# Performance work log

Hardware: AMD Instinct MI355X
Metric: run time of the kernel (lower is better)

The kernel has to match this reference:

```python
import jax, jax.numpy as jnp
import numpy as np

B, N_BUG, D_BUG, K, L, P = 2048, 2000, 30, 20, 40, 2
OMEGA_TEMP = 1.0


def setup_inputs() -> dict:
    key = jax.random.key(0)
    ks = jax.random.split(key, 14)
    f = lambda k, s, sc=1.0: sc * jax.random.normal(k, s, dtype=jnp.float32)
    return {
        "x": f(ks[0], (B, N_BUG)),
        "microbe_locs": f(ks[1], (N_BUG, D_BUG)),
        "mu_bug": f(ks[2], (L, D_BUG)),
        "r_bug": jax.random.uniform(ks[3], (L,), dtype=jnp.float32) * 20.0 + 10.0,
        "alpha": f(ks[4], (L, K)),
        "beta": f(ks[5], (K,)),
        "W1": f(ks[6], (K, L, P, 16), 0.5),
        "b1": f(ks[7], (K, L, P, 16), 0.1),
        "W2": f(ks[8], (K, L, P, 16, 16), 0.25),
        "b2": f(ks[9], (K, L, P, 16), 0.1),
        "W3": f(ks[10], (K, L, P, 16, 8), 0.25),
        "b3": f(ks[11], (K, L, P, 8), 0.1),
        "W4": f(ks[12], (K, L, P, 8), 0.35),
        "b4": f(ks[13], (K, L, P), 0.1),
    }


def reference(x, microbe_locs, mu_bug, r_bug, alpha, beta,
              W1, b1, W2, b2, W3, b3, W4, b4):
    # Distance-based soft microbe->cluster assignment (mu/r kernel):
    # kappa[m,l] = ||microbe_locs[m] - mu_bug[l]||^2
    kappa = jnp.sum((microbe_locs[:, None, :] - mu_bug[None, :, :]) ** 2, axis=-1)  # [N_bug, L]
    w_act = jax.nn.sigmoid((r_bug[None, :] - kappa) / OMEGA_TEMP)                  # [N_bug, L]
    g = x @ w_act                                                                   # [B, L] per-cluster microbe sums

    alpha_act = jax.nn.sigmoid(alpha)  # [L, K] soft edge selection

    # NAM: K*L*P independent tiny MLPs 1->16->16->8->1, batched over (k,l,p).
    h1 = jax.nn.elu(g[:, None, :, None, None] * W1[None] + b1[None])          # [B,K,L,P,16]
    h2 = jax.nn.elu(jnp.einsum('bklpi,klpij->bklpj', h1, W2) + b2[None])      # [B,K,L,P,16]
    h3 = jax.nn.elu(jnp.einsum('bklpi,klpij->bklpj', h2, W3) + b3[None])      # [B,K,L,P,8]
    f_out = jnp.einsum('bklpi,klpi->bklp', h3, W4) + b4[None]                 # [B,K,L,P]

    # out[b,k] = beta[k] + sum_l alpha_act[l,k] * sum_p f_out[b,k,l,p]
    out = beta[None, :] + jnp.einsum('bklp,lk->bk', f_out, alpha_act)         # [B,K]
    return out
```

## Files before the change

### kernel.cpp

```cpp
#include <hip/hip_runtime.h>
#include <hip/hip_bf16.h>

#define B_SZ 2048
#define NB   2000
#define DB   30
#define KK   20
#define LL   40
#define PP   2

#define BLOB_F 336

#define GRID_K1 880

typedef _Float16 f16x4 __attribute__((ext_vector_type(4)));
typedef float    f32x4 __attribute__((ext_vector_type(4)));

__device__ __forceinline__ float sigmoidf_fast(float z) {
    return 1.0f / (1.0f + __expf(-z));
}
__device__ __forceinline__ float eluf(float x) {
    return x > 0.0f ? x : (__expf(x) - 1.0f);
}

__global__ __launch_bounds__(256) void k1_prep(
    const float* __restrict__ locs, const float* __restrict__ mu,
    const float* __restrict__ r, const float* __restrict__ alpha,
    const float* __restrict__ beta,
    const float* __restrict__ W1, const float* __restrict__ b1,
    const float* __restrict__ W2, const float* __restrict__ b2,
    const float* __restrict__ W3, const float* __restrict__ b3,
    const float* __restrict__ W4, const float* __restrict__ b4,
    float* __restrict__ w_act, float* __restrict__ blob,
    float* __restrict__ g_T, float* __restrict__ out)
{
    __shared__ float smem[LL * DB + LL];
    const int tid  = threadIdx.x;
    const int bidx = blockIdx.x;
    const int vt   = bidx * 256 + tid;

    for (int j = vt; j < LL * B_SZ; j += GRID_K1 * 256) g_T[j] = 0.0f;

    if (bidx < 320) {
        for (int t = tid; t < LL * DB; t += 256) smem[t] = mu[t];
        if (tid < LL) smem[LL * DB + tid] = r[tid];
        __syncthreads();
        if (vt < NB * LL) {
            int m = vt / LL;
            int l = vt - m * LL;
            float kappa = 0.0f;
            #pragma unroll
            for (int d = 0; d < DB; ++d) {
                float diff = locs[m * DB + d] - smem[l * DB + d];
                kappa += diff * diff;
            }
            w_act[vt] = sigmoidf_fast(smem[LL * DB + l] - kappa);
        }
    } else if (bidx < 720) {
        int vt2 = vt - 320 * 256;
        int bidb = vt2 >> 6;
        int t = vt2 & 63;
        int k = bidb / (PP * LL);
        int rem = bidb - k * (PP * LL);
        int p = rem / LL;
        int l = rem - p * LL;
        int iw = (k * LL + l) * PP + p;
        int n = t & 15, q = t >> 4;
        float* o = blob + (size_t)bidb * BLOB_F;
        float aact = sigmoidf_fast(alpha[l * KK + k]);
        if (t < 16) {
            o[t]      = W1[iw * 16 + t];
            o[16 + t] = b1[iw * 16 + t];
            o[32 + t] = b2[iw * 16 + t];
            o[48 + t] = (t < 8) ? b3[iw * 8 + t] : 0.0f;
            o[64 + t] = (t < 8) ? W4[iw * 8 + t] * aact : 0.0f;
        }
        _Float16* w2a = (_Float16*)(o + 80);
        #pragma unroll
        for (int j = 0; j < 4; ++j)
            w2a[t * 4 + j] = (_Float16)W2[iw * 256 + (4 * q + j) * 16 + n];
        _Float16* w3a = (_Float16*)(o + 208);
        #pragma unroll
        for (int j = 0; j < 4; ++j)
            w3a[t * 4 + j] = (n < 8) ? (_Float16)W3[iw * 128 + (4 * q + j) * 8 + n]
                                     : (_Float16)0.0f;
    } else {
        if (tid < KK) {
            int k = tid;
            float s = beta[k];
            for (int l = 0; l < LL; ++l) {
                float a = sigmoidf_fast(alpha[l * KK + k]);
                s += a * (b4[(k * LL + l) * PP + 0] + b4[(k * LL + l) * PP + 1]);
            }
            smem[tid] = s;
        }
        __syncthreads();
        int gid = (bidx - 720) * 256 + tid;
        out[gid] = smem[gid % KK];
    }
}

__global__ __launch_bounds__(256) void k2_g(
    const float* __restrict__ x,
    const float* __restrict__ w_act,
    float* __restrict__ g_T)
{
    __shared__ float xs[64 * 125];

    int bb = blockIdx.x >> 4;
    int mq = blockIdx.x & 15;
    int tid = threadIdx.x;
    int i = tid & 63;
    int wu = __builtin_amdgcn_readfirstlane(tid >> 6);

    for (int t = tid; t < 64 * 125; t += 256) {
        int ii = t / 125;
        int jj = t - ii * 125;
        xs[t] = x[(bb * 64 + ii) * NB + mq * 125 + jj];
    }
    __syncthreads();

    const float* wrow = w_act + (mq * 125) * LL + wu * 10;
    const float* xrow = xs + i * 125;

    float acc[10];
    #pragma unroll
    for (int u = 0; u < 10; ++u) acc[u] = 0.0f;

    #pragma unroll 5
    for (int m = 0; m < 125; ++m) {
        float xv = xrow[m];
        #pragma unroll
        for (int u = 0; u < 10; ++u)
            acc[u] = fmaf(xv, wrow[m * LL + u], acc[u]);
    }

    #pragma unroll
    for (int u = 0; u < 10; ++u)
        atomicAdd(&g_T[(wu * 10 + u) * B_SZ + bb * 64 + i], acc[u]);
}

__global__ __launch_bounds__(256) void k3_nam(
    const float* __restrict__ g_T,
    const float* __restrict__ blob,
    float* __restrict__ out)
{
    __shared__ __align__(16) float sw[10 * BLOB_F];

    int bid = blockIdx.x;
    int bb = bid & 15;
    int lc = (bid >> 4) & 3;
    int p  = (bid >> 6) & 1;
    int k  = bid >> 7;
    int tid = threadIdx.x;

    const int wv = tid >> 6, lane = tid & 63;
    const int n = lane & 15, q = lane >> 4;
    int b0 = bb * 128 + wv * 32 + n;

    float gv0[10], gv1[10];
    #pragma unroll
    for (int u = 0; u < 10; ++u) {
        gv0[u] = g_T[(lc * 10 + u) * B_SZ + b0];
        gv1[u] = g_T[(lc * 10 + u) * B_SZ + b0 + 16];
    }

    {
        const float4* bl4 = (const float4*)blob;
        float4* sw4 = (float4*)sw;
        int base = ((k * PP + p) * LL + lc * 10) * (BLOB_F / 4);
        for (int t = tid; t < 10 * (BLOB_F / 4); t += 256)
            sw4[t] = bl4[base + t];
    }
    __syncthreads();

    float acc0 = 0.0f, acc1 = 0.0f;

    #pragma unroll 1
    for (int u = 0; u < 10; ++u) {
        const float* W = sw + u * BLOB_F;
        f32x4 w1q = *(const f32x4*)(W + q * 4);
        f32x4 b1q = *(const f32x4*)(W + 16 + q * 4);
        f32x4 b2q = *(const f32x4*)(W + 32 + q * 4);
        f32x4 b3q = *(const f32x4*)(W + 48 + q * 4);
        f32x4 w4q = *(const f32x4*)(W + 64 + q * 4);
        f16x4 w2a = *(const f16x4*)((const _Float16*)(W + 80) + lane * 4);
        f16x4 w3a = *(const f16x4*)((const _Float16*)(W + 208) + lane * 4);

        float g0 = gv0[u];
        float g1 = gv1[u];

        f16x4 hb0, hb1;
        #pragma unroll
        for (int j = 0; j < 4; ++j) {
            hb0[j] = (_Float16)eluf(fmaf(g0, w1q[j], b1q[j]));
            hb1[j] = (_Float16)eluf(fmaf(g1, w1q[j], b1q[j]));
        }

        f32x4 d20 = __builtin_amdgcn_mfma_f32_16x16x16f16(w2a, hb0, b2q, 0, 0, 0);
        f32x4 d21 = __builtin_amdgcn_mfma_f32_16x16x16f16(w2a, hb1, b2q, 0, 0, 0);

        f16x4 hc0, hc1;
        #pragma unroll
        for (int j = 0; j < 4; ++j) {
            hc0[j] = (_Float16)eluf(d20[j]);
            hc1[j] = (_Float16)eluf(d21[j]);
        }

        f32x4 d30 = __builtin_amdgcn_mfma_f32_16x16x16f16(w3a, hc0, b3q, 0, 0, 0);
        f32x4 d31 = __builtin_amdgcn_mfma_f32_16x16x16f16(w3a, hc1, b3q, 0, 0, 0);

        #pragma unroll
        for (int rj = 0; rj < 4; ++rj) {
            acc0 = fmaf(eluf(d30[rj]), w4q[rj], acc0);
            acc1 = fmaf(eluf(d31[rj]), w4q[rj], acc1);
        }
    }

    acc0 += __shfl_xor(acc0, 16, 64);
    acc0 += __shfl_xor(acc0, 32, 64);
    acc1 += __shfl_xor(acc1, 16, 64);
    acc1 += __shfl_xor(acc1, 32, 64);
    if (lane < 16) {
        atomicAdd(&out[b0 * KK + k], acc0);
        atomicAdd(&out[(b0 + 16) * KK + k], acc1);
    }
}

extern "C" void kernel_launch(void* const* d_in, const int* in_sizes, int n_in,
                              void* d_out, int out_size, void* d_ws, size_t ws_size,
                              hipStream_t stream) {
    const float* x     = (const float*)d_in[0];
    const float* locs  = (const float*)d_in[1];
    const float* mu    = (const float*)d_in[2];
    const float* r     = (const float*)d_in[3];
    const float* alpha = (const float*)d_in[4];
    const float* beta  = (const float*)d_in[5];
    const float* W1    = (const float*)d_in[6];
    const float* b1    = (const float*)d_in[7];
    const float* W2    = (const float*)d_in[8];
    const float* b2    = (const float*)d_in[9];
    const float* W3    = (const float*)d_in[10];
    const float* b3    = (const float*)d_in[11];
    const float* W4    = (const float*)d_in[12];
    const float* b4    = (const float*)d_in[13];
    float* out = (float*)d_out;

    float* ws0   = (float*)d_ws;
    float* w_act = ws0;
    float* g_T   = w_act + NB * LL;
    float* blob  = g_T + LL * B_SZ;

    k1_prep<<<GRID_K1, 256, 0, stream>>>(locs, mu, r, alpha, beta,
                                         W1, b1, W2, b2, W3, b3, W4, b4,
                                         w_act, blob, g_T, out);
    k2_g<<<512, 256, 0, stream>>>(x, w_act, g_T);
    k3_nam<<<2560, 256, 0, stream>>>(g_T, blob, out);
}
```

Before: 146.0 us.

## Use packed half2 ELU, coarsen NAM blocks over two outputs, and regroup prep kernels

The first two ELU layers of the NAM kernel now run in packed fp16 arithmetic, using min, exp2 and max on half2 values instead of per-element fp32 expf with a branch. Each NAM block now handles two output columns k, so the g values loaded into registers are reused across both and the grid is halved. Shared memory per block doubles to hold both weight sets. The preparation work is regrouped: the weight-blob packing and output initialisation now run in the same launch as the x·w_act reduction instead of in the first kernel. The fp16 ELU lowers the precision of the hidden activations somewhat.

```diff
diff --git a/kernel.cpp b/kernel.cpp
--- a/kernel.cpp
+++ b/kernel.cpp
@@ -1,5 +1,4 @@
 #include <hip/hip_runtime.h>
-#include <hip/hip_bf16.h>
 
 #define B_SZ 2048
 #define NB   2000
@@ -10,10 +9,11 @@
 
 #define BLOB_F 336
 
-#define GRID_K1 880
-
 typedef _Float16 f16x4 __attribute__((ext_vector_type(4)));
+typedef _Float16 f16x2 __attribute__((ext_vector_type(2)));
 typedef float    f32x4 __attribute__((ext_vector_type(4)));
+
+union F16x4 { f16x4 v; f16x2 h[2]; };
 
 __device__ __forceinline__ float sigmoidf_fast(float z) {
     return 1.0f / (1.0f + __expf(-z));
@@ -21,42 +21,93 @@
 __device__ __forceinline__ float eluf(float x) {
     return x > 0.0f ? x : (__expf(x) - 1.0f);
 }
-
-__global__ __launch_bounds__(256) void k1_prep(
+__device__ __forceinline__ f16x2 elu2(f16x2 x) {
+    const f16x2 z2  = {(_Float16)0.0f, (_Float16)0.0f};
+    const f16x2 l2e = {(_Float16)1.4426950408889634f, (_Float16)1.4426950408889634f};
+    const f16x2 m1  = {(_Float16)-1.0f, (_Float16)-1.0f};
+    f16x2 e = __builtin_elementwise_exp2(__builtin_elementwise_min(x, z2) * l2e);
+    return __builtin_elementwise_max(x, e + m1);
+}
+__device__ __forceinline__ f16x2 pack2(float a, float b) {
+    f16x2 r = {(_Float16)a, (_Float16)b};
+    return r;
+}
+
+__global__ __launch_bounds__(256) void k1_wact(
     const float* __restrict__ locs, const float* __restrict__ mu,
-    const float* __restrict__ r, const float* __restrict__ alpha,
-    const float* __restrict__ beta,
+    const float* __restrict__ r,
+    float* __restrict__ w_act, float* __restrict__ g_T)
+{
+    __shared__ float smem[LL * DB + LL];
+    const int tid = threadIdx.x;
+    const int vt  = blockIdx.x * 256 + tid;
+
+    g_T[vt] = 0.0f;
+
+    for (int t = tid; t < LL * DB; t += 256) smem[t] = mu[t];
+    if (tid < LL) smem[LL * DB + tid] = r[tid];
+    __syncthreads();
+    if (vt < NB * LL) {
+        int m = vt / LL;
+        int l = vt - m * LL;
+        float kappa = 0.0f;
+        #pragma unroll
+        for (int d = 0; d < DB; ++d) {
+            float diff = locs[m * DB + d] - smem[l * DB + d];
+            kappa += diff * diff;
+        }
+        w_act[vt] = sigmoidf_fast(smem[LL * DB + l] - kappa);
+    }
+}
+
+__global__ __launch_bounds__(256) void k2_mix(
+    const float* __restrict__ x,
+    const float* __restrict__ w_act,
+    const float* __restrict__ alpha, const float* __restrict__ beta,
     const float* __restrict__ W1, const float* __restrict__ b1,
     const float* __restrict__ W2, const float* __restrict__ b2,
     const float* __restrict__ W3, const float* __restrict__ b3,
     const float* __restrict__ W4, const float* __restrict__ b4,
-    float* __restrict__ w_act, float* __restrict__ blob,
-    float* __restrict__ g_T, float* __restrict__ out)
+    float* __restrict__ g_T,
+    float* __restrict__ blob, float* __restrict__ out)
 {
-    __shared__ float smem[LL * DB + LL];
+    __shared__ float xs[64 * 125];
+    const int bidx = blockIdx.x;
     const int tid  = threadIdx.x;
-    const int bidx = blockIdx.x;
-    const int vt   = bidx * 256 + tid;
-
-    for (int j = vt; j < LL * B_SZ; j += GRID_K1 * 256) g_T[j] = 0.0f;
-
-    if (bidx < 320) {
-        for (int t = tid; t < LL * DB; t += 256) smem[t] = mu[t];
-        if (tid < LL) smem[LL * DB + tid] = r[tid];
+
+    if (bidx < 512) {
+        int bb = bidx >> 4;
+        int mq = bidx & 15;
+        int i  = tid & 63;
+        int wu = __builtin_amdgcn_readfirstlane(tid >> 6);
+
+        for (int t = tid; t < 64 * 125; t += 256) {
+            int ii = t / 125;
+            int jj = t - ii * 125;
+            xs[t] = x[(bb * 64 + ii) * NB + mq * 125 + jj];
+        }
         __syncthreads();
-        if (vt < NB * LL) {
-            int m = vt / LL;
-            int l = vt - m * LL;
-            float kappa = 0.0f;
+
+        const float* wrow = w_act + (mq * 125) * LL + wu * 10;
+        const float* xrow = xs + i * 125;
+
+        float acc[10];
+        #pragma unroll
+        for (int u = 0; u < 10; ++u) acc[u] = 0.0f;
+
+        #pragma unroll 5
+        for (int m = 0; m < 125; ++m) {
+            float xv = xrow[m];
             #pragma unroll
-            for (int d = 0; d < DB; ++d) {
-                float diff = locs[m * DB + d] - smem[l * DB + d];
-                kappa += diff * diff;
-            }
-            w_act[vt] = sigmoidf_fast(smem[LL * DB + l] - kappa);
-        }
-    } else if (bidx < 720) {
-        int vt2 = vt - 320 * 256;
+            for (int u = 0; u < 10; ++u)
+                acc[u] = fmaf(xv, wrow[m * LL + u], acc[u]);
+        }
+
+        #pragma unroll
+        for (int u = 0; u < 10; ++u)
+            atomicAdd(&g_T[(wu * 10 + u) * B_SZ + bb * 64 + i], acc[u]);
+    } else if (bidx < 912) {
+        int vt2 = (bidx - 512) * 256 + tid;
         int bidb = vt2 >> 6;
         int t = vt2 & 63;
         int k = bidb / (PP * LL);
@@ -91,52 +142,12 @@
                 float a = sigmoidf_fast(alpha[l * KK + k]);
                 s += a * (b4[(k * LL + l) * PP + 0] + b4[(k * LL + l) * PP + 1]);
             }
-            smem[tid] = s;
+            xs[tid] = s;
         }
         __syncthreads();
-        int gid = (bidx - 720) * 256 + tid;
-        out[gid] = smem[gid % KK];
-    }
-}
-
-__global__ __launch_bounds__(256) void k2_g(
-    const float* __restrict__ x,
-    const float* __restrict__ w_act,
-    float* __restrict__ g_T)
-{
-    __shared__ float xs[64 * 125];
-
-    int bb = blockIdx.x >> 4;
-    int mq = blockIdx.x & 15;
-    int tid = threadIdx.x;
-    int i = tid & 63;
-    int wu = __builtin_amdgcn_readfirstlane(tid >> 6);
-
-    for (int t = tid; t < 64 * 125; t += 256) {
-        int ii = t / 125;
-        int jj = t - ii * 125;
-        xs[t] = x[(bb * 64 + ii) * NB + mq * 125 + jj];
-    }
-    __syncthreads();
-
-    const float* wrow = w_act + (mq * 125) * LL + wu * 10;
-    const float* xrow = xs + i * 125;
-
-    float acc[10];
-    #pragma unroll
-    for (int u = 0; u < 10; ++u) acc[u] = 0.0f;
-
-    #pragma unroll 5
-    for (int m = 0; m < 125; ++m) {
-        float xv = xrow[m];
-        #pragma unroll
-        for (int u = 0; u < 10; ++u)
-            acc[u] = fmaf(xv, wrow[m * LL + u], acc[u]);
-    }
-
-    #pragma unroll
-    for (int u = 0; u < 10; ++u)
-        atomicAdd(&g_T[(wu * 10 + u) * B_SZ + bb * 64 + i], acc[u]);
+        int gid = (bidx - 912) * 256 + tid;
+        out[gid] = xs[gid % KK];
+    }
 }
 
 __global__ __launch_bounds__(256) void k3_nam(
@@ -144,13 +155,13 @@
     const float* __restrict__ blob,
     float* __restrict__ out)
 {
-    __shared__ __align__(16) float sw[10 * BLOB_F];
+    __shared__ __align__(16) float sw[2][10 * BLOB_F];
 
     int bid = blockIdx.x;
     int bb = bid & 15;
     int lc = (bid >> 4) & 3;
     int p  = (bid >> 6) & 1;
-    int k  = bid >> 7;
+    int kp = bid >> 7;
     int tid = threadIdx.x;
 
     const int wv = tid >> 6, lane = tid & 63;
@@ -167,62 +178,71 @@
     {
         const float4* bl4 = (const float4*)blob;
         float4* sw4 = (float4*)sw;
-        int base = ((k * PP + p) * LL + lc * 10) * (BLOB_F / 4);
-        for (int t = tid; t < 10 * (BLOB_F / 4); t += 256)
-            sw4[t] = bl4[base + t];
+        int base0 = (((2 * kp + 0) * PP + p) * LL + lc * 10) * (BLOB_F / 4);
+        int base1 = (((2 * kp + 1) * PP + p) * LL + lc * 10) * (BLOB_F / 4);
+        for (int t = tid; t < 10 * (BLOB_F / 4); t += 256) {
+            sw4[t] = bl4[base0 + t];
+            sw4[10 * (BLOB_F / 4) + t] = bl4[base1 + t];
+        }
     }
     __syncthreads();
 
-    float acc0 = 0.0f, acc1 = 0.0f;
-
     #pragma unroll 1
-    for (int u = 0; u < 10; ++u) {
-        const float* W = sw + u * BLOB_F;
-        f32x4 w1q = *(const f32x4*)(W + q * 4);
-        f32x4 b1q = *(const f32x4*)(W + 16 + q * 4);
-        f32x4 b2q = *(const f32x4*)(W + 32 + q * 4);
-        f32x4 b3q = *(const f32x4*)(W + 48 + q * 4);
-        f32x4 w4q = *(const f32x4*)(W + 64 + q * 4);
-        f16x4 w2a = *(const f16x4*)((const _Float16*)(W + 80) + lane * 4);
-        f16x4 w3a = *(const f16x4*)((const _Float16*)(W + 208) + lane * 4);
-
-        float g0 = gv0[u];
-        float g1 = gv1[u];
-
-        f16x4 hb0, hb1;
-        #pragma unroll
-        for (int j = 0; j < 4; ++j) {
-            hb0[j] = (_Float16)eluf(fmaf(g0, w1q[j], b1q[j]));
-            hb1[j] = (_Float16)eluf(fmaf(g1, w1q[j], b1q[j]));
-        }
-
-        f32x4 d20 = __builtin_amdgcn_mfma_f32_16x16x16f16(w2a, hb0, b2q, 0, 0, 0);
-        f32x4 d21 = __builtin_amdgcn_mfma_f32_16x16x16f16(w2a, hb1, b2q, 0, 0, 0);
-
-        f16x4 hc0, hc1;
-        #pragma unroll
-        for (int j = 0; j < 4; ++j) {
-            hc0[j] = (_Float16)eluf(d20[j]);
-            hc1[j] = (_Float16)eluf(d21[j]);
-        }
-
-        f32x4 d30 = __builtin_amdgcn_mfma_f32_16x16x16f16(w3a, hc0, b3q, 0, 0, 0);
-        f32x4 d31 = __builtin_amdgcn_mfma_f32_16x16x16f16(w3a, hc1, b3q, 0, 0, 0);
-
-        #pragma unroll
-        for (int rj = 0; rj < 4; ++rj) {
-            acc0 = fmaf(eluf(d30[rj]), w4q[rj], acc0);
-            acc1 = fmaf(eluf(d31[rj]), w4q[rj], acc1);
-        }
-    }
-
-    acc0 += __shfl_xor(acc0, 16, 64);
-    acc0 += __shfl_xor(acc0, 32, 64);
-    acc1 += __shfl_xor(acc1, 16, 64);
-    acc1 += __shfl_xor(acc1, 32, 64);
-    if (lane < 16) {
-        atomicAdd(&out[b0 * KK + k], acc0);
-        atomicAdd(&out[(b0 + 16) * KK + k], acc1);
+    for (int kk = 0; kk < 2; ++kk) {
+        float acc0 = 0.0f, acc1 = 0.0f;
+
+        #pragma unroll 1
+        for (int u = 0; u < 10; ++u) {
+            const float* W = sw[kk] + u * BLOB_F;
+            f32x4 w1q = *(const f32x4*)(W + q * 4);
+            f32x4 b1q = *(const f32x4*)(W + 16 + q * 4);
+            f32x4 b2q = *(const f32x4*)(W + 32 + q * 4);
+            f32x4 b3q = *(const f32x4*)(W + 48 + q * 4);
+            f32x4 w4q = *(const f32x4*)(W + 64 + q * 4);
+            f16x4 w2a = *(const f16x4*)((const _Float16*)(W + 80) + lane * 4);
+            f16x4 w3a = *(const f16x4*)((const _Float16*)(W + 208) + lane * 4);
+
+            float g0 = gv0[u];
+            float g1 = gv1[u];
+
+            F16x4 hb0, hb1;
+            hb0.h[0] = elu2(pack2(fmaf(g0, w1q[0], b1q[0]),
+                                  fmaf(g0, w1q[1], b1q[1])));
+            hb0.h[1] = elu2(pack2(fmaf(g0, w1q[2], b1q[2]),
+                                  fmaf(g0, w1q[3], b1q[3])));
+            hb1.h[0] = elu2(pack2(fmaf(g1, w1q[0], b1q[0]),
+                                  fmaf(g1, w1q[1], b1q[1])));
+            hb1.h[1] = elu2(pack2(fmaf(g1, w1q[2], b1q[2]),
+                                  fmaf(g1, w1q[3], b1q[3])));
+
+            f32x4 d20 = __builtin_amdgcn_mfma_f32_16x16x16f16(w2a, hb0.v, b2q, 0, 0, 0);
+            f32x4 d21 = __builtin_amdgcn_mfma_f32_16x16x16f16(w2a, hb1.v, b2q, 0, 0, 0);
+
+            F16x4 hc0, hc1;
+            hc0.h[0] = elu2(pack2(d20[0], d20[1]));
+            hc0.h[1] = elu2(pack2(d20[2], d20[3]));
+            hc1.h[0] = elu2(pack2(d21[0], d21[1]));
+            hc1.h[1] = elu2(pack2(d21[2], d21[3]));
+
+            f32x4 d30 = __builtin_amdgcn_mfma_f32_16x16x16f16(w3a, hc0.v, b3q, 0, 0, 0);
+            f32x4 d31 = __builtin_amdgcn_mfma_f32_16x16x16f16(w3a, hc1.v, b3q, 0, 0, 0);
+
+            #pragma unroll
+            for (int rj = 0; rj < 4; ++rj) {
+                acc0 = fmaf(eluf(d30[rj]), w4q[rj], acc0);
+                acc1 = fmaf(eluf(d31[rj]), w4q[rj], acc1);
+            }
+        }
+
+        acc0 += __shfl_xor(acc0, 16, 64);
+        acc0 += __shfl_xor(acc0, 32, 64);
+        acc1 += __shfl_xor(acc1, 16, 64);
+        acc1 += __shfl_xor(acc1, 32, 64);
+        if (lane < 16) {
+            int k = 2 * kp + kk;
+            atomicAdd(&out[b0 * KK + k], acc0);
+            atomicAdd(&out[(b0 + 16) * KK + k], acc1);
+        }
     }
 }
 
@@ -250,9 +270,9 @@
     float* g_T   = w_act + NB * LL;
     float* blob  = g_T + LL * B_SZ;
 
-    k1_prep<<<GRID_K1, 256, 0, stream>>>(locs, mu, r, alpha, beta,
-                                         W1, b1, W2, b2, W3, b3, W4, b4,
-                                         w_act, blob, g_T, out);
-    k2_g<<<512, 256, 0, stream>>>(x, w_act, g_T);
-    k3_nam<<<2560, 256, 0, stream>>>(g_T, blob, out);
-}
+    k1_wact<<<320, 256, 0, stream>>>(locs, mu, r, w_act, g_T);
+    k2_mix<<<1072, 256, 0, stream>>>(x, w_act, alpha, beta,
+                                     W1, b1, W2, b2, W3, b3, W4, b4,
+                                     g_T, blob, out);
+    k3_nam<<<1280, 256, 0, stream>>>(g_T, blob, out);
+}
```

Measured after the change: 144.5 us. No clear change (-1.0%).
